# Performance work log

Measured on AMD Instinct MI355X. Metric: run time of the kernel, lower is better.

Reference implementation:

```python
import jax, jax.numpy as jnp
import numpy as np

KERNEL_SIZE = 7
NUM_HEADS = 16
CHANNELS = 1024
HEAD_DIM = CHANNELS // NUM_HEADS
PAD = KERNEL_SIZE // 2


def setup_inputs() -> dict:
    key = jax.random.key(0)
    k1, k2 = jax.random.split(key)
    B, S, C = 4, 2048, CHANNELS
    x = jax.random.normal(k1, (B, S, C), dtype=jnp.float32)
    W_pred = jax.random.normal(k2, (C, KERNEL_SIZE * NUM_HEADS), dtype=jnp.float32) * (1.0 / np.sqrt(C))
    b_pred = jnp.zeros((KERNEL_SIZE * NUM_HEADS,), dtype=jnp.float32)
    return {"x": x, "W_pred": W_pred, "b_pred": b_pred}


def reference(x, W_pred, b_pred):
    B, S, C = x.shape
    # per-position kernel prediction: [B,S,H,K]
    kernels = (jnp.einsum('bsc,ck->bsk', x, W_pred) + b_pred).reshape(B, S, NUM_HEADS, KERNEL_SIZE)
    # split channels into heads: [B,S,H,D]
    x_heads = x.reshape(B, S, NUM_HEADS, HEAD_DIM)
    # pad along sequence dim
    x_pad = jnp.pad(x_heads, ((0, 0), (PAD, PAD), (0, 0), (0, 0)))
    # sum over K shifted slices weighted by predicted kernels (K is small, fixed)
    out = jnp.zeros_like(x_heads)
    for i in range(KERNEL_SIZE):
        out = out + kernels[:, :, :, i:i + 1] * jax.lax.dynamic_slice_in_dim(x_pad, i, S, axis=1)
    return out.reshape(B, S, C)
```

## Files before the change

kernel.cpp:

```cpp
#include <hip/hip_runtime.h>
#include <hip/hip_bf16.h>
#include <cstdint>

#define SEQ   2048
#define CH    1024
#define NHEAD 16
#define HDIM  64
#define KSZ   7
#define NCOL  112
#define PADW  3

#define BM       32
#define BK       64
#define NTHREADS 256
#define LDA_STR  72
#define LDB_STR  72
#define LDK_STR  113

typedef __bf16 v8bf __attribute__((ext_vector_type(8)));
typedef float  v4f  __attribute__((ext_vector_type(4)));

__global__ __launch_bounds__(NTHREADS)
void dynconv_fused(const float* __restrict__ x,
                   const float* __restrict__ Wp,
                   const float* __restrict__ bp,
                   float* __restrict__ out)
{
    __shared__ __bf16 ldsA[BM * LDA_STR];
    __shared__ __bf16 ldsB[NCOL * LDB_STR];
    __shared__ float  ldsK[BM * LDK_STR];

    const int tid = threadIdx.x;
    const int bb  = blockIdx.x;
    const int b   = bb >> 6;
    const int s0  = (bb & 63) << 5;

    const int wave = tid >> 6;
    const int lane = tid & 63;
    const int lq   = lane >> 4;
    const int lm   = lane & 15;

    const int stripe = wave & 1;
    const int t0     = (wave >> 1) * 4;
    const int nt     = (wave >> 1) ? 3 : 4;

    v4f acc[4];
    acc[0] = (v4f){0.f,0.f,0.f,0.f};
    acc[1] = (v4f){0.f,0.f,0.f,0.f};
    acc[2] = (v4f){0.f,0.f,0.f,0.f};
    acc[3] = (v4f){0.f,0.f,0.f,0.f};

    const float* xbase = x + (size_t)b * SEQ * CH;
    const float* xrow0 = xbase + (size_t)s0 * CH;

    for (int kc = 0; kc < CH; kc += BK) {
        #pragma unroll
        for (int j = 0; j < 2; ++j) {
            const int q  = j * NTHREADS + tid;
            const int r  = q >> 4;
            const int k4 = (q & 15) << 2;
            const v4f v = *(const v4f*)(xrow0 + (size_t)r * CH + kc + k4);
            __bf16* d = &ldsA[r * LDA_STR + k4];
            d[0] = (__bf16)v.x; d[1] = (__bf16)v.y; d[2] = (__bf16)v.z; d[3] = (__bf16)v.w;
        }
        #pragma unroll
        for (int j = 0; j < 7; ++j) {
            const int q  = j * NTHREADS + tid;
            const int kk = q / 28;
            const int n4 = (q - kk * 28) << 2;
            const v4f v = *(const v4f*)(Wp + (size_t)(kc + kk) * NCOL + n4);
            ldsB[(n4 + 0) * LDB_STR + kk] = (__bf16)v.x;
            ldsB[(n4 + 1) * LDB_STR + kk] = (__bf16)v.y;
            ldsB[(n4 + 2) * LDB_STR + kk] = (__bf16)v.z;
            ldsB[(n4 + 3) * LDB_STR + kk] = (__bf16)v.w;
        }
        __syncthreads();

        #pragma unroll
        for (int ks = 0; ks < BK; ks += 32) {
            const v8bf afrag = *(const v8bf*)&ldsA[(stripe * 16 + lm) * LDA_STR + ks + lq * 8];
            for (int t = 0; t < nt; ++t) {
                const v8bf bfrag = *(const v8bf*)&ldsB[((t0 + t) * 16 + lm) * LDB_STR + ks + lq * 8];
                acc[t] = __builtin_amdgcn_mfma_f32_16x16x32_bf16(afrag, bfrag, acc[t], 0, 0, 0);
            }
        }
        __syncthreads();
    }

    for (int t = 0; t < nt; ++t) {
        const int col  = (t0 + t) * 16 + lm;
        const float bias = bp[col];
        #pragma unroll
        for (int r = 0; r < 4; ++r) {
            const int row = stripe * 16 + lq * 4 + r;
            ldsK[row * LDK_STR + col] = acc[t][r] + bias;
        }
    }
    __syncthreads();

    const int h  = tid >> 4;
    const int c4 = tid << 2;
    float* orow0 = out + ((size_t)b * SEQ + s0) * CH;

    v4f win[7];
    #pragma unroll
    for (int i = 0; i < 6; ++i) {
        const int sg = s0 - PADW + i;
        win[i] = (sg >= 0 && sg < SEQ) ? *(const v4f*)(xbase + (size_t)sg * CH + c4)
                                       : (v4f){0.f,0.f,0.f,0.f};
    }
    win[6] = (v4f){0.f,0.f,0.f,0.f};

    #pragma unroll
    for (int r = 0; r < BM; ++r) {
        const int sg = s0 + r + PADW;
        win[6] = (sg < SEQ) ? *(const v4f*)(xbase + (size_t)sg * CH + c4)
                            : (v4f){0.f,0.f,0.f,0.f};

        const float* kp = &ldsK[r * LDK_STR + h * KSZ];
        v4f a = (v4f){0.f,0.f,0.f,0.f};
        #pragma unroll
        for (int i = 0; i < 7; ++i) {
            a += kp[i] * win[i];
        }
        *(v4f*)(orow0 + (size_t)r * CH + c4) = a;

        #pragma unroll
        for (int i = 0; i < 6; ++i) win[i] = win[i + 1];
    }
}

extern "C" void kernel_launch(void* const* d_in, const int* in_sizes, int n_in,
                              void* d_out, int out_size, void* d_ws, size_t ws_size,
                              hipStream_t stream) {
    const float* x  = (const float*)d_in[0];
    const float* Wp = (const float*)d_in[1];
    const float* bp = (const float*)d_in[2];
    float* out = (float*)d_out;
    dynconv_fused<<<dim3(256), dim3(NTHREADS), 0, stream>>>(x, Wp, bp, out);
}
```

Before: 128.7 us.

## Pre-swizzle weights into MFMA fragments, halve row tile, drop LDS staging for GEMM

A new prep kernel converts W_pred to bf16 and lays it out in MFMA B-fragment order in the workspace. The main kernel then loads A and B fragments straight from global memory, with no LDS staging and no per-chunk barriers. The row tile shrinks from 32 to 16, which doubles the grid to 512 blocks, and the 4 waves split the 7 column tiles between them. The convolution window is preloaded into registers before the barrier to overlap with the GEMM epilogue. In exchange there is an extra kernel launch, more global traffic for the weight fragments across blocks, and higher register pressure from the 22-entry window.

Result: faster. 105.2 us (-18.3%).

```diff
diff --git a/kernel.cpp b/kernel.cpp
--- a/kernel.cpp
+++ b/kernel.cpp
@@ -5,128 +5,128 @@
 #define SEQ   2048
 #define CH    1024
 #define NHEAD 16
-#define HDIM  64
 #define KSZ   7
 #define NCOL  112
 #define PADW  3
 
-#define BM       32
-#define BK       64
+#define BM       16
 #define NTHREADS 256
-#define LDA_STR  72
-#define LDB_STR  72
 #define LDK_STR  113
+#define NKSTEP   32
+#define WS_FRAG_BYTES (NKSTEP * 7 * 64 * 16)
 
 typedef __bf16 v8bf __attribute__((ext_vector_type(8)));
 typedef float  v4f  __attribute__((ext_vector_type(4)));
 
-__global__ __launch_bounds__(NTHREADS)
+__global__ __launch_bounds__(256)
+void prep_w(const float* __restrict__ Wp, __bf16* __restrict__ wsB) {
+    const int g  = blockIdx.x * 256 + threadIdx.x;
+    const int j  = g & 7;
+    const int l  = (g >> 3) & 63;
+    const int st = g >> 9;
+    const int s  = st / 7;
+    const int t  = st - s * 7;
+    const int k  = s * 32 + (l >> 4) * 8 + j;
+    const int n  = t * 16 + (l & 15);
+    wsB[g] = (__bf16)Wp[k * NCOL + n];
+}
+
+template <bool PRE>
+__global__ __launch_bounds__(NTHREADS, 2)
 void dynconv_fused(const float* __restrict__ x,
                    const float* __restrict__ Wp,
                    const float* __restrict__ bp,
+                   const __bf16* __restrict__ wsB,
                    float* __restrict__ out)
 {
-    __shared__ __bf16 ldsA[BM * LDA_STR];
-    __shared__ __bf16 ldsB[NCOL * LDB_STR];
-    __shared__ float  ldsK[BM * LDK_STR];
+    __shared__ float ldsK[BM * LDK_STR];
 
-    const int tid = threadIdx.x;
-    const int bb  = blockIdx.x;
-    const int b   = bb >> 6;
-    const int s0  = (bb & 63) << 5;
+    const int tid  = threadIdx.x;
+    const int bb   = blockIdx.x;
+    const int b    = bb >> 7;
+    const int s0   = (bb & 127) << 4;
 
     const int wave = tid >> 6;
     const int lane = tid & 63;
     const int lq   = lane >> 4;
     const int lm   = lane & 15;
 
-    const int stripe = wave & 1;
-    const int t0     = (wave >> 1) * 4;
-    const int nt     = (wave >> 1) ? 3 : 4;
+    const float* xbase = x + (size_t)b * SEQ * CH;
 
-    v4f acc[4];
-    acc[0] = (v4f){0.f,0.f,0.f,0.f};
-    acc[1] = (v4f){0.f,0.f,0.f,0.f};
-    acc[2] = (v4f){0.f,0.f,0.f,0.f};
-    acc[3] = (v4f){0.f,0.f,0.f,0.f};
+    const int tile0 = wave * 2;
+    const int tile1 = (wave < 3) ? wave * 2 + 1 : 6;
 
-    const float* xbase = x + (size_t)b * SEQ * CH;
-    const float* xrow0 = xbase + (size_t)s0 * CH;
+    v4f acc0 = (v4f){0.f, 0.f, 0.f, 0.f};
+    v4f acc1 = (v4f){0.f, 0.f, 0.f, 0.f};
 
-    for (int kc = 0; kc < CH; kc += BK) {
-        #pragma unroll
-        for (int j = 0; j < 2; ++j) {
-            const int q  = j * NTHREADS + tid;
-            const int r  = q >> 4;
-            const int k4 = (q & 15) << 2;
-            const v4f v = *(const v4f*)(xrow0 + (size_t)r * CH + kc + k4);
-            __bf16* d = &ldsA[r * LDA_STR + k4];
-            d[0] = (__bf16)v.x; d[1] = (__bf16)v.y; d[2] = (__bf16)v.z; d[3] = (__bf16)v.w;
-        }
-        #pragma unroll
-        for (int j = 0; j < 7; ++j) {
-            const int q  = j * NTHREADS + tid;
-            const int kk = q / 28;
-            const int n4 = (q - kk * 28) << 2;
-            const v4f v = *(const v4f*)(Wp + (size_t)(kc + kk) * NCOL + n4);
-            ldsB[(n4 + 0) * LDB_STR + kk] = (__bf16)v.x;
-            ldsB[(n4 + 1) * LDB_STR + kk] = (__bf16)v.y;
-            ldsB[(n4 + 2) * LDB_STR + kk] = (__bf16)v.z;
-            ldsB[(n4 + 3) * LDB_STR + kk] = (__bf16)v.w;
-        }
-        __syncthreads();
+    const float* arow = xbase + (size_t)(s0 + lm) * CH + lq * 8;
 
-        #pragma unroll
-        for (int ks = 0; ks < BK; ks += 32) {
-            const v8bf afrag = *(const v8bf*)&ldsA[(stripe * 16 + lm) * LDA_STR + ks + lq * 8];
-            for (int t = 0; t < nt; ++t) {
-                const v8bf bfrag = *(const v8bf*)&ldsB[((t0 + t) * 16 + lm) * LDB_STR + ks + lq * 8];
-                acc[t] = __builtin_amdgcn_mfma_f32_16x16x32_bf16(afrag, bfrag, acc[t], 0, 0, 0);
+    #pragma unroll 8
+    for (int s = 0; s < NKSTEP; ++s) {
+        const float* p = arow + s * 32;
+        const v4f v0 = *(const v4f*)p;
+        const v4f v1 = *(const v4f*)(p + 4);
+        v8bf af;
+        af[0] = (__bf16)v0.x; af[1] = (__bf16)v0.y;
+        af[2] = (__bf16)v0.z; af[3] = (__bf16)v0.w;
+        af[4] = (__bf16)v1.x; af[5] = (__bf16)v1.y;
+        af[6] = (__bf16)v1.z; af[7] = (__bf16)v1.w;
+
+        v8bf bf0, bf1;
+        if (PRE) {
+            bf0 = *(const v8bf*)&wsB[(size_t)((s * 7 + tile0) * 64 + lane) * 8];
+            bf1 = *(const v8bf*)&wsB[(size_t)((s * 7 + tile1) * 64 + lane) * 8];
+        } else {
+            #pragma unroll
+            for (int j = 0; j < 8; ++j) {
+                const int k = s * 32 + lq * 8 + j;
+                bf0[j] = (__bf16)Wp[k * NCOL + tile0 * 16 + lm];
+                bf1[j] = (__bf16)Wp[k * NCOL + tile1 * 16 + lm];
             }
         }
-        __syncthreads();
+        acc0 = __builtin_amdgcn_mfma_f32_16x16x32_bf16(af, bf0, acc0, 0, 0, 0);
+        acc1 = __builtin_amdgcn_mfma_f32_16x16x32_bf16(af, bf1, acc1, 0, 0, 0);
     }
 
-    for (int t = 0; t < nt; ++t) {
-        const int col  = (t0 + t) * 16 + lm;
-        const float bias = bp[col];
+    {
+        const int ct0 = tile0 * 16 + lm;
+        const float bias0 = bp[ct0];
         #pragma unroll
-        for (int r = 0; r < 4; ++r) {
-            const int row = stripe * 16 + lq * 4 + r;
-            ldsK[row * LDK_STR + col] = acc[t][r] + bias;
+        for (int r = 0; r < 4; ++r)
+            ldsK[(lq * 4 + r) * LDK_STR + ct0] = acc0[r] + bias0;
+        if (wave < 3) {
+            const int ct1 = tile1 * 16 + lm;
+            const float bias1 = bp[ct1];
+            #pragma unroll
+            for (int r = 0; r < 4; ++r)
+                ldsK[(lq * 4 + r) * LDK_STR + ct1] = acc1[r] + bias1;
         }
     }
-    __syncthreads();
 
     const int h  = tid >> 4;
     const int c4 = tid << 2;
-    float* orow0 = out + ((size_t)b * SEQ + s0) * CH;
 
-    v4f win[7];
+    v4f win[BM + 6];
     #pragma unroll
-    for (int i = 0; i < 6; ++i) {
+    for (int i = 0; i < BM + 6; ++i) {
         const int sg = s0 - PADW + i;
-        win[i] = (sg >= 0 && sg < SEQ) ? *(const v4f*)(xbase + (size_t)sg * CH + c4)
-                                       : (v4f){0.f,0.f,0.f,0.f};
+        win[i] = (sg >= 0 && sg < SEQ)
+                     ? *(const v4f*)(xbase + (size_t)sg * CH + c4)
+                     : (v4f){0.f, 0.f, 0.f, 0.f};
     }
-    win[6] = (v4f){0.f,0.f,0.f,0.f};
 
+    __syncthreads();
+
+    float* orow = out + ((size_t)b * SEQ + s0) * CH + c4;
     #pragma unroll
     for (int r = 0; r < BM; ++r) {
-        const int sg = s0 + r + PADW;
-        win[6] = (sg < SEQ) ? *(const v4f*)(xbase + (size_t)sg * CH + c4)
-                            : (v4f){0.f,0.f,0.f,0.f};
-
         const float* kp = &ldsK[r * LDK_STR + h * KSZ];
-        v4f a = (v4f){0.f,0.f,0.f,0.f};
+        v4f a = (v4f){0.f, 0.f, 0.f, 0.f};
         #pragma unroll
-        for (int i = 0; i < 7; ++i) {
-            a += kp[i] * win[i];
+        for (int i = 0; i < KSZ; ++i) {
+            a += kp[i] * win[r + i];
         }
-        *(v4f*)(orow0 + (size_t)r * CH + c4) = a;
-
-        #pragma unroll
-        for (int i = 0; i < 6; ++i) win[i] = win[i + 1];
+        *(v4f*)(orow + (size_t)r * CH) = a;
     }
 }
 
@@ -137,5 +137,12 @@
     const float* Wp = (const float*)d_in[1];
     const float* bp = (const float*)d_in[2];
     float* out = (float*)d_out;
-    dynconv_fused<<<dim3(256), dim3(NTHREADS), 0, stream>>>(x, Wp, bp, out);
+
+    if (ws_size >= (size_t)WS_FRAG_BYTES) {
+        __bf16* wsB = (__bf16*)d_ws;
+        prep_w<<<dim3(448), dim3(256), 0, stream>>>(Wp, wsB);
+        dynconv_fused<true><<<dim3(512), dim3(NTHREADS), 0, stream>>>(x, Wp, bp, wsB, out);
+    } else {
+        dynconv_fused<false><<<dim3(512), dim3(NTHREADS), 0, stream>>>(x, Wp, bp, nullptr, out);
+    }
 }
```
